# Performance work log

Hardware: AMD Instinct MI355X
Metric: run time of the kernel (lower is better)

The kernel has to match this reference:

```python
import jax, jax.numpy as jnp
import numpy as np

H = 300          # node_hidden_dim (GINE output dim)
D = 2 * H        # set2set in_channels = 600
STEPS = 2        # num_step_set2_set


def _lstm_cell(x, h, c, W_ih, W_hh, b_ih, b_hh):
    # PyTorch LSTM gate order: i, f, g, o
    gates = x @ W_ih.T + h @ W_hh.T + b_ih + b_hh
    i, f, g, o = jnp.split(gates, 4, axis=-1)
    c = jax.nn.sigmoid(f) * c + jax.nn.sigmoid(i) * jnp.tanh(g)
    h = jax.nn.sigmoid(o) * jnp.tanh(c)
    return h, c


def _set2set(x, batch, num_graphs, W_ih, W_hh, b_ih, b_hh):
    # torch_geometric Set2Set with processing_steps=STEPS, 1-layer LSTM
    B = num_graphs
    q_star = jnp.zeros((B, 2 * D), x.dtype)
    h = jnp.zeros((B, D), x.dtype)
    c = jnp.zeros((B, D), x.dtype)
    for _ in range(STEPS):
        h, c = _lstm_cell(q_star, h, c, W_ih, W_hh, b_ih, b_hh)
        q = h                                   # [B, D]
        e = jnp.sum(x * q[batch], axis=-1)      # [N]
        emax = jax.ops.segment_max(e, batch, num_segments=B)
        a = jnp.exp(e - emax[batch])
        asum = jax.ops.segment_sum(a, batch, num_segments=B)
        a = a / (asum[batch] + 1e-16)           # segment softmax
        r = jax.ops.segment_sum(a[:, None] * x, batch, num_segments=B)
        q_star = jnp.concatenate([q, r], axis=-1)   # [B, 2D]
    return q_star


def _l2norm(x):
    return x / jnp.maximum(jnp.linalg.norm(x, axis=1, keepdims=True), 1e-12)


def setup_inputs() -> dict:
    key = jax.random.key(0)
    ks = jax.random.split(key, 8)
    Nu, Nv, B = 8192, 8192, 256
    solute_x = jax.random.normal(ks[0], (Nu, H), jnp.float32)
    solvent_x = jax.random.normal(ks[1], (Nv, H), jnp.float32)
    solute_batch = jnp.sort(jax.random.randint(ks[2], (Nu,), 0, B)).astype(jnp.int32)
    solvent_batch = jnp.sort(jax.random.randint(ks[3], (Nv,), 0, B)).astype(jnp.int32)
    lstm_W_ih = jax.random.normal(ks[4], (4 * D, 2 * D), jnp.float32) * 0.02
    lstm_W_hh = jax.random.normal(ks[5], (4 * D, D), jnp.float32) * 0.02
    lstm_b_ih = jnp.zeros((4 * D,), jnp.float32)
    lstm_b_hh = jnp.zeros((4 * D,), jnp.float32)
    pred_W = jax.random.normal(ks[6], (1, 8 * H), jnp.float32) * 0.02
    pred_b = jnp.zeros((1,), jnp.float32)
    return {
        "solute_x": solute_x, "solvent_x": solvent_x,
        "solute_batch": solute_batch, "solvent_batch": solvent_batch,
        "num_graphs": B,
        "lstm_W_ih": lstm_W_ih, "lstm_W_hh": lstm_W_hh,
        "lstm_b_ih": lstm_b_ih, "lstm_b_hh": lstm_b_hh,
        "pred_W": pred_W, "pred_b": pred_b,
    }


def reference(solute_x, solvent_x, solute_batch, solvent_batch, num_graphs,
              lstm_W_ih, lstm_W_hh, lstm_b_ih, lstm_b_hh, pred_W, pred_b):
    # F.normalize(dim=1)
    su = _l2norm(solute_x)    # [Nu, H]
    sv = _l2norm(solvent_x)   # [Nv, H]
    # len_map = solute_len.T @ solvent_len == same-pair membership mask
    mask = (solute_batch[:, None] == solvent_batch[None, :]).astype(su.dtype)
    interaction_map = (su @ sv.T) * mask          # [Nu, Nv]
    ret_interaction_map = interaction_map
    solvent_prime = interaction_map.T @ su        # [Nv, H]
    solute_prime = interaction_map @ sv           # [Nu, H]
    su2 = jnp.concatenate([su, solute_prime], axis=1)    # [Nu, 2H]
    sv2 = jnp.concatenate([sv, solvent_prime], axis=1)   # [Nv, 2H]
    su_s2s = _set2set(su2, solute_batch, num_graphs, lstm_W_ih, lstm_W_hh, lstm_b_ih, lstm_b_hh)
    sv_s2s = _set2set(sv2, solvent_batch, num_graphs, lstm_W_ih, lstm_W_hh, lstm_b_ih, lstm_b_hh)
    final = jnp.concatenate([su_s2s, sv_s2s], axis=1)    # [B, 8H]
    predictions = final @ pred_W.T + pred_b              # [B, 1]
    return predictions, ret_interaction_map
```

## Files before the change

kernel.cpp:

```cpp
#include <hip/hip_runtime.h>
#include <math.h>

#define HDIM 300
#define DDIM 600
#define NGR  256

typedef float vf4 __attribute__((ext_vector_type(4)));
typedef float vf2 __attribute__((ext_vector_type(2)));

__device__ __forceinline__ float wred_sum(float v){
  #pragma unroll
  for(int o=32;o;o>>=1) v += __shfl_xor(v,o,64);
  return v;
}
__device__ __forceinline__ float wred_max(float v){
  #pragma unroll
  for(int o=32;o;o>>=1) v = fmaxf(v,__shfl_xor(v,o,64));
  return v;
}
__device__ __forceinline__ float sigm(float x){ return 1.f/(1.f+expf(-x)); }

__device__ __forceinline__ void fill_row(int i, const int* __restrict__ ub,
    const int* __restrict__ voff, float* __restrict__ mapbase, int Nv, int tid){
  int g = ub[i];
  int js = voff[g], je = voff[g+1];
  float* mrow = mapbase + (size_t)i*Nv;
  const vf4 z4 = {0.f,0.f,0.f,0.f};
  int nf4 = Nv >> 2;
  for (int q4=tid; q4<nf4; q4+=256){
    int j0 = q4*4;
    if (j0+4 <= js || j0 >= je){
      __builtin_nontemporal_store(z4, (vf4*)(mrow + j0));
    } else {
      #pragma unroll
      for(int u=0;u<4;u++){ int j=j0+u; if (j<js || j>=je) mrow[j]=0.f; }
    }
  }
}

__global__ __launch_bounds__(256) void k_norm_off(const float* __restrict__ xu,
    const float* __restrict__ xv, float* __restrict__ su, float* __restrict__ sv,
    int Nu, int Nv, const int* __restrict__ ub, const int* __restrict__ vb,
    int* __restrict__ uoff, int* __restrict__ voff,
    const float* __restrict__ b_ih, const float* __restrict__ b_hh,
    float* __restrict__ h1, float* __restrict__ c1,
    const float* __restrict__ pb, float* __restrict__ outp,
    const float* __restrict__ Wih, const float* __restrict__ Whh,
    float* __restrict__ gbase){
  int NBn = (Nu + Nv) >> 2;
  int b = blockIdx.x;
  int tid = threadIdx.x, lane = tid & 63, w = tid >> 6;
  if (b == NBn){
    int t = tid;
    if (t < NGR){
      int lo=0, hi=Nu;
      while(lo<hi){ int m=(lo+hi)>>1; if (ub[m] < t) lo=m+1; else hi=m; }
      uoff[t]=lo;
      lo=0; hi=Nv;
      while(lo<hi){ int m=(lo+hi)>>1; if (vb[m] < t) lo=m+1; else hi=m; }
      voff[t]=lo;
      if (t==0){ uoff[NGR]=Nu; voff[NGR]=Nv; }
      outp[t] = pb[0];
    }
    for (int d=tid; d<DDIM; d+=256){
      float gi = b_ih[d]      + b_hh[d];
      float gg = b_ih[1200+d] + b_hh[1200+d];
      float go = b_ih[1800+d] + b_hh[1800+d];
      float c  = sigm(gi)*tanhf(gg);
      c1[d]=c; h1[d]=sigm(go)*tanhf(c);
    }
    return;
  }
  if (b > NBn){
    __shared__ float h1l[DDIM];
    for (int d=tid; d<DDIM; d+=256){
      float gi = b_ih[d]      + b_hh[d];
      float gg = b_ih[1200+d] + b_hh[1200+d];
      float go = b_ih[1800+d] + b_hh[1800+d];
      float c  = sigm(gi)*tanhf(gg);
      h1l[d]   = sigm(go)*tanhf(c);
    }
    __syncthreads();
    int n = (b - NBn - 1)*4 + w;
    const float* wi = Wih + (size_t)n*1200;
    const float* wh = Whh + (size_t)n*600;
    float s = 0.f;
    for (int k=lane; k<DDIM; k+=64) s += h1l[k]*(wi[k] + wh[k]);
    s = wred_sum(s);
    if (lane==0) gbase[n] = s + b_ih[n] + b_hh[n];
    return;
  }
  int wid = b*4 + w;
  const float* src; float* dst;
  if (wid < Nu){ src = xu + (size_t)wid*HDIM; dst = su + (size_t)wid*HDIM; }
  else         { src = xv + (size_t)(wid-Nu)*HDIM; dst = sv + (size_t)(wid-Nu)*HDIM; }
  const vf4* s4 = (const vf4*)src;
  vf4 A = s4[lane];
  vf4 Bv = (lane<11)? s4[64+lane] : (vf4){0.f,0.f,0.f,0.f};
  float s = A.x*A.x+A.y*A.y+A.z*A.z+A.w*A.w + Bv.x*Bv.x+Bv.y*Bv.y+Bv.z*Bv.z+Bv.w*Bv.w;
  s = wred_sum(s);
  float inv = 1.f / fmaxf(sqrtf(s), 1e-12f);
  vf4* d4 = (vf4*)dst;
  d4[lane] = A*inv;
  if (lane<11) d4[64+lane] = Bv*inv;
}

__global__ __launch_bounds__(256) void k_prime(const float* __restrict__ su,
    const float* __restrict__ sv, const int* __restrict__ ub,
    const int* __restrict__ vb, const int* __restrict__ uoff,
    const int* __restrict__ voff, float* __restrict__ spr,
    float* __restrict__ svp, float* __restrict__ e1u, float* __restrict__ e1v,
    const float* __restrict__ h1, float* __restrict__ mapbase, int Nu, int Nv){
  int b = blockIdx.x;
  int tid = threadIdx.x, lane = tid & 63, w = tid >> 6;
  int r = b % 3;
  if (r == 2){ fill_row(b/3, ub, voff, mapbase, Nv, tid); return; }
  int idx = (b/3)*2 + r;
  bool isU = (idx < Nu);
  int i = isU ? idx : idx - Nu;
  const float* xa = isU ? su : sv;
  const float* xb = isU ? sv : su;
  const int* mybatch = isU ? ub : vb;
  const int* ooff    = isU ? voff : uoff;
  float* prime = isU ? spr : svp;
  float* eout  = isU ? e1u : e1v;

  __shared__ __align__(16) float xrow[304];
  __shared__ __align__(16) float prl[4*304];
  __shared__ float qv[2*HDIM];
  __shared__ float red[4];
  const float* rowp = xa + (size_t)i*HDIM;
  for (int t=tid; t<HDIM;   t+=256) xrow[t] = rowp[t];
  for (int t=tid; t<2*HDIM; t+=256) qv[t]   = h1[t];
  int g = mybatch[i];
  int js = ooff[g], je = ooff[g+1];
  __syncthreads();

  const vf4* x4 = (const vf4*)xrow;
  vf4 xA = x4[lane];
  vf4 xB = (lane<11)? x4[64+lane] : (vf4){0.f,0.f,0.f,0.f};
  vf4 prA = {0.f,0.f,0.f,0.f}, prB = {0.f,0.f,0.f,0.f};
  for (int j = js + w; j < je; j += 4){
    const vf4* orow = (const vf4*)(xb + (size_t)j*HDIM);
    vf4 oA = orow[lane];
    vf4 oB = (lane<11)? orow[64+lane] : (vf4){0.f,0.f,0.f,0.f};
    float d = oA.x*xA.x + oA.y*xA.y + oA.z*xA.z + oA.w*xA.w
            + oB.x*xB.x + oB.y*xB.y + oB.z*xB.z + oB.w*xB.w;
    d = wred_sum(d);
    if (isU && lane==0) mapbase[(size_t)i*Nv + j] = d;
    prA += d * oA;
    prB += d * oB;
  }
  vf4* p4 = (vf4*)(prl + w*304);
  p4[lane] = prA;
  if (lane<11) p4[64+lane] = prB;
  __syncthreads();
  float ep = 0.f;
  for (int t=tid; t<HDIM; t+=256){
    float s = prl[t] + prl[304+t] + prl[608+t] + prl[912+t];
    prime[(size_t)i*HDIM + t] = s;
    ep += xrow[t]*qv[t] + s*qv[HDIM+t];
  }
  ep = wred_sum(ep);
  if (lane==0) red[w] = ep;
  __syncthreads();
  if (tid==0) eout[i] = red[0]+red[1]+red[2]+red[3];
}

__global__ __launch_bounds__(256) void k_r1(const float* __restrict__ su,
    const float* __restrict__ sv, const float* __restrict__ spr,
    const float* __restrict__ svp, const float* __restrict__ e1u,
    const float* __restrict__ e1v, const int* __restrict__ uoff,
    const int* __restrict__ voff, float* __restrict__ r1){
  int tid = threadIdx.x, lane = tid & 63, w = tid >> 6;
  int bs = blockIdx.x; int set = bs >> 8; int g = bs & 255;
  const float* x  = set? sv  : su;
  const float* pr = set? svp : spr;
  const float* e  = set? e1v : e1u;
  const int* off  = set? voff: uoff;
  __shared__ float al[2048]; __shared__ float red[4]; __shared__ float shv;
  int ns = off[g], ne = off[g+1]; int n = ne - ns;
  float m = -INFINITY;
  for (int t=ns+tid; t<ne; t+=256) m = fmaxf(m, e[t]);
  m = wred_max(m);
  if (lane==0) red[w]=m;
  __syncthreads();
  if (tid==0) shv = fmaxf(fmaxf(red[0],red[1]),fmaxf(red[2],red[3]));
  __syncthreads();
  float emax = shv;
  float s = 0.f;
  for (int t=tid; t<n; t+=256){ float a = expf(e[ns+t]-emax); if (t<2048) al[t]=a; s += a; }
  s = wred_sum(s);
  __syncthreads();
  if (lane==0) red[w]=s;
  __syncthreads();
  if (tid==0) shv = red[0]+red[1]+red[2]+red[3];
  __syncthreads();
  float inv = 1.f/(shv + 1e-16f);
  float acc[3] = {0.f,0.f,0.f};
  for (int nn=0; nn<n; nn++){
    float a = (nn<2048)? al[nn] : expf(e[ns+nn]-emax);
    const float* xr = x  + (size_t)(ns+nn)*HDIM;
    const float* pp = pr + (size_t)(ns+nn)*HDIM;
    #pragma unroll
    for(int u=0;u<3;u++){ int c = tid + u*256; if (c<DDIM){
        float xv = (c<HDIM)? xr[c] : pp[c-HDIM]; acc[u] += a*xv; } }
  }
  #pragma unroll
  for(int u=0;u<3;u++){ int c = tid + u*256; if (c<DDIM) r1[(size_t)bs*DDIM + c] = acc[u]*inv; }
}

__global__ __launch_bounds__(256) void k_gemm_lstm(const float* __restrict__ r1,
    const float* __restrict__ Wih, const float* __restrict__ gbase,
    const float* __restrict__ c1, float* __restrict__ h2){
  __shared__ __align__(16) float smem[32*68];
  float* Al = smem;
  float* Bl = smem + 16*36;
  int tid = threadIdx.x;
  int d0  = blockIdx.x*16;
  int gs0 = blockIdx.y*32;
  int tx = tid & 15, ty = tid >> 4;
  float acc[2][4] = {};
  for (int kt=0; kt<600; kt+=16){
    int k = kt + tx;
    bool kok = (k < 600);
    #pragma unroll
    for (int u=0; u<2; u++){
      int rl = ty + u*16;
      Al[tx*36 + rl] = kok ? r1[(size_t)(gs0+rl)*DDIM + k] : 0.f;
    }
    #pragma unroll
    for (int u=0; u<4; u++){
      int cl = ty + u*16;
      int gate = cl >> 4, dd = cl & 15;
      int d = d0 + dd;
      Bl[tx*68 + cl] = (kok && d < 600)
          ? Wih[(size_t)(gate*600 + d)*1200 + 600 + k] : 0.f;
    }
    __syncthreads();
    #pragma unroll
    for (int kk=0; kk<16; kk++){
      vf2 av = ((const vf2*)(Al + kk*36))[ty];
      vf4 bv = ((const vf4*)(Bl + kk*68))[tx];
      float a[2]={av.x,av.y}, bb[4]={bv.x,bv.y,bv.z,bv.w};
      #pragma unroll
      for(int mm=0;mm<2;mm++)
        #pragma unroll
        for(int nn=0;nn<4;nn++) acc[mm][nn] += a[mm]*bb[nn];
    }
    __syncthreads();
  }
  #pragma unroll
  for (int mm=0; mm<2; mm++){
    vf4 o = {acc[mm][0], acc[mm][1], acc[mm][2], acc[mm][3]};
    ((vf4*)(smem + (ty*2+mm)*68))[tx] = o;
  }
  __syncthreads();
  int d_l = tid & 15, r0 = tid >> 4;
  int d = d0 + d_l;
  if (d < 600){
    float gb_i = gbase[d], gb_f = gbase[600+d], gb_g = gbase[1200+d], gb_o = gbase[1800+d];
    float cc1 = c1[d];
    #pragma unroll
    for (int u=0; u<2; u++){
      int rl = r0 + u*16;
      const float* gr = smem + rl*68;
      float gi = gr[d_l]      + gb_i;
      float gf = gr[16+d_l]   + gb_f;
      float gG = gr[32+d_l]   + gb_g;
      float go = gr[48+d_l]   + gb_o;
      float c  = sigm(gf)*cc1 + sigm(gi)*tanhf(gG);
      h2[(size_t)(gs0+rl)*DDIM + d] = sigm(go)*tanhf(c);
    }
  }
}

__global__ __launch_bounds__(256) void k_r2(const float* __restrict__ su,
    const float* __restrict__ sv, const float* __restrict__ spr,
    const float* __restrict__ svp, const int* __restrict__ uoff,
    const int* __restrict__ voff, const float* __restrict__ h2,
    const float* __restrict__ pW, float* __restrict__ e2u,
    float* __restrict__ e2v, float* __restrict__ outp){
  int tid = threadIdx.x, lane = tid & 63, w = tid >> 6;
  int bs = blockIdx.x; int set = bs >> 8; int g = bs & 255;
  const float* x  = set? sv  : su;
  const float* pr = set? svp : spr;
  const int* off  = set? voff: uoff;
  float* e2g      = set? e2v : e2u;
  __shared__ float q[DDIM]; __shared__ float e2l[128]; __shared__ float al[128];
  __shared__ float red[4]; __shared__ float shv;
  for (int t=tid; t<DDIM; t+=256) q[t] = h2[(size_t)bs*DDIM + t];
  int ns = off[g], ne = off[g+1]; int n = ne - ns;
  __syncthreads();
  for (int node = ns + w; node < ne; node += 4){
    const float* xr = x  + (size_t)node*HDIM;
    const float* pp = pr + (size_t)node*HDIM;
    float d = 0.f;
    #pragma unroll
    for(int c=0;c<10;c++){ int k = lane + 64*c; if (k<DDIM){
        float xv = (k<HDIM)? xr[k] : pp[k-HDIM]; d += xv*q[k]; } }
    d = wred_sum(d);
    if (lane==0){ int t = node-ns; if (t<128) e2l[t] = d; else e2g[node] = d; }
  }
  __syncthreads();
  float m = -INFINITY;
  for (int t=tid; t<n; t+=256) m = fmaxf(m, (t<128)? e2l[t] : e2g[ns+t]);
  m = wred_max(m);
  if (lane==0) red[w]=m;
  __syncthreads();
  if (tid==0) shv = fmaxf(fmaxf(red[0],red[1]),fmaxf(red[2],red[3]));
  __syncthreads();
  float emax = shv;
  float s = 0.f;
  for (int t=tid; t<n; t+=256){
    float a = expf(((t<128)? e2l[t] : e2g[ns+t]) - emax);
    if (t<128) al[t]=a; else e2g[ns+t]=a;
    s += a;
  }
  s = wred_sum(s);
  __syncthreads();
  if (lane==0) red[w]=s;
  __syncthreads();
  if (tid==0) shv = red[0]+red[1]+red[2]+red[3];
  __syncthreads();
  float inv = 1.f/(shv + 1e-16f);
  float acc[3] = {0.f,0.f,0.f};
  for (int nn=0; nn<n; nn++){
    float a = (nn<128)? al[nn] : e2g[ns+nn];
    const float* xr = x  + (size_t)(ns+nn)*HDIM;
    const float* pp = pr + (size_t)(ns+nn)*HDIM;
    #pragma unroll
    for(int u=0;u<3;u++){ int c = tid + u*256; if (c<DDIM){
        float xv = (c<HDIM)? xr[c] : pp[c-HDIM]; acc[u] += a*xv; } }
  }
  int hoff = set? 1200 : 0;
  float p = 0.f;
  #pragma unroll
  for(int u=0;u<3;u++){ int c = tid + u*256; if (c<DDIM) p += (acc[u]*inv)*pW[hoff+600+c]; }
  for (int t=tid; t<DDIM; t+=256) p += q[t]*pW[hoff+t];
  p = wred_sum(p);
  __syncthreads();
  if (lane==0) red[w] = p;
  __syncthreads();
  if (tid==0) atomicAdd(&outp[g], red[0]+red[1]+red[2]+red[3]);
}

extern "C" void kernel_launch(void* const* d_in, const int* in_sizes, int n_in,
                              void* d_out, int out_size, void* d_ws, size_t ws_size,
                              hipStream_t stream) {
  const float* solute_x  = (const float*)d_in[0];
  const float* solvent_x = (const float*)d_in[1];
  const int*   ub        = (const int*)d_in[2];
  const int*   vb        = (const int*)d_in[3];
  const float* Wih  = (const float*)d_in[5];
  const float* Whh  = (const float*)d_in[6];
  const float* b_ih = (const float*)d_in[7];
  const float* b_hh = (const float*)d_in[8];
  const float* pW   = (const float*)d_in[9];
  const float* pb   = (const float*)d_in[10];

  int Nu = in_sizes[0] / HDIM;
  int Nv = in_sizes[1] / HDIM;

  float* out = (float*)d_out;
  int predn = out_size - Nu*Nv;
  float* mapbase = out + predn;

  float* ws = (float*)d_ws;
  float* su    = ws;
  float* sv    = su    + (size_t)Nu*HDIM;
  float* spr   = sv    + (size_t)Nv*HDIM;
  float* svp   = spr   + (size_t)Nu*HDIM;
  float* e1u   = svp   + (size_t)Nv*HDIM;
  float* e1v   = e1u   + Nu;
  float* h1    = e1v   + Nv;
  float* c1    = h1    + DDIM;
  float* r1    = c1    + DDIM;
  float* gbase = r1    + 512*DDIM;
  float* h2    = gbase + 2400;
  int*   uoff  = (int*)(h2 + 512*DDIM);
  int*   voff  = uoff + 257;

  k_norm_off<<<dim3((Nu+Nv)/4 + 1 + 600), dim3(256), 0, stream>>>(
      solute_x, solvent_x, su, sv, Nu, Nv, ub, vb, uoff, voff,
      b_ih, b_hh, h1, c1, pb, out, Wih, Whh, gbase);
  k_prime<<<dim3(24576), dim3(256), 0, stream>>>(
      su, sv, ub, vb, uoff, voff, spr, svp, e1u, e1v, h1, mapbase, Nu, Nv);
  k_r1<<<dim3(512), dim3(256), 0, stream>>>(
      su, sv, spr, svp, e1u, e1v, uoff, voff, r1);
  k_gemm_lstm<<<dim3(38, 16), dim3(256), 0, stream>>>(r1, Wih, gbase, c1, h2);
  k_r2<<<dim3(512), dim3(256), 0, stream>>>(
      su, sv, spr, svp, uoff, voff, h2, pW, e1u, e1v, out);
}
```

Baseline: 524.6 us.

## Spread interaction-map zero-fill rows across prime, r1 and r2 kernels

Before, the 8192 zero-fill rows of the interaction map were all interleaved into k_prime. Now k_prime fills 5461 rows, and the remaining rows are split between k_r1 and k_r2 as extra blocks, assigned with a proportional interleaving helper. The aim is to hide the bandwidth-bound map writes behind the small, latency-bound r1 and r2 kernels, which launch only 512 blocks each. The cost is extra blocks in those kernels and a risk of contending with their memory traffic.

```diff
diff --git a/kernel.cpp b/kernel.cpp
--- a/kernel.cpp
+++ b/kernel.cpp
@@ -36,6 +36,13 @@
       for(int u=0;u<4;u++){ int j=j0+u; if (j<js || j>=je) mrow[j]=0.f; }
     }
   }
+}
+
+__device__ __forceinline__ int split_cf(int b, int C, int G, int* fi){
+  unsigned ci = (unsigned)(((unsigned long long)b * (unsigned)C) / (unsigned)G);
+  unsigned cn = (unsigned)(((unsigned long long)(b+1) * (unsigned)C) / (unsigned)G);
+  if (cn == ci){ *fi = b - (int)ci; return -1; }
+  return (int)ci;
 }
 
 __global__ __launch_bounds__(256) void k_norm_off(const float* __restrict__ xu,
@@ -111,11 +118,10 @@
     const int* __restrict__ voff, float* __restrict__ spr,
     float* __restrict__ svp, float* __restrict__ e1u, float* __restrict__ e1v,
     const float* __restrict__ h1, float* __restrict__ mapbase, int Nu, int Nv){
-  int b = blockIdx.x;
   int tid = threadIdx.x, lane = tid & 63, w = tid >> 6;
-  int r = b % 3;
-  if (r == 2){ fill_row(b/3, ub, voff, mapbase, Nv, tid); return; }
-  int idx = (b/3)*2 + r;
+  int fi;
+  int idx = split_cf(blockIdx.x, 16384, 21845, &fi);
+  if (idx < 0){ fill_row(fi, ub, voff, mapbase, Nv, tid); return; }
   bool isU = (idx < Nu);
   int i = isU ? idx : idx - Nu;
   const float* xa = isU ? su : sv;
@@ -171,9 +177,13 @@
     const float* __restrict__ sv, const float* __restrict__ spr,
     const float* __restrict__ svp, const float* __restrict__ e1u,
     const float* __restrict__ e1v, const int* __restrict__ uoff,
-    const int* __restrict__ voff, float* __restrict__ r1){
+    const int* __restrict__ voff, float* __restrict__ r1,
+    const int* __restrict__ ub, float* __restrict__ mapbase, int Nv){
   int tid = threadIdx.x, lane = tid & 63, w = tid >> 6;
-  int bs = blockIdx.x; int set = bs >> 8; int g = bs & 255;
+  int fi;
+  int bs = split_cf(blockIdx.x, 512, 1877, &fi);
+  if (bs < 0){ fill_row(5461 + fi, ub, voff, mapbase, Nv, tid); return; }
+  int set = bs >> 8; int g = bs & 255;
   const float* x  = set? sv  : su;
   const float* pr = set? svp : spr;
   const float* e  = set? e1v : e1u;
@@ -280,9 +290,13 @@
     const float* __restrict__ svp, const int* __restrict__ uoff,
     const int* __restrict__ voff, const float* __restrict__ h2,
     const float* __restrict__ pW, float* __restrict__ e2u,
-    float* __restrict__ e2v, float* __restrict__ outp){
+    float* __restrict__ e2v, float* __restrict__ outp,
+    const int* __restrict__ ub, float* __restrict__ mapbase, int Nv){
   int tid = threadIdx.x, lane = tid & 63, w = tid >> 6;
-  int bs = blockIdx.x; int set = bs >> 8; int g = bs & 255;
+  int fi;
+  int bs = split_cf(blockIdx.x, 512, 1878, &fi);
+  if (bs < 0){ fill_row(6826 + fi, ub, voff, mapbase, Nv, tid); return; }
+  int set = bs >> 8; int g = bs & 255;
   const float* x  = set? sv  : su;
   const float* pr = set? svp : spr;
   const int* off  = set? voff: uoff;
@@ -384,11 +398,11 @@
   k_norm_off<<<dim3((Nu+Nv)/4 + 1 + 600), dim3(256), 0, stream>>>(
       solute_x, solvent_x, su, sv, Nu, Nv, ub, vb, uoff, voff,
       b_ih, b_hh, h1, c1, pb, out, Wih, Whh, gbase);
-  k_prime<<<dim3(24576), dim3(256), 0, stream>>>(
+  k_prime<<<dim3(21845), dim3(256), 0, stream>>>(
       su, sv, ub, vb, uoff, voff, spr, svp, e1u, e1v, h1, mapbase, Nu, Nv);
-  k_r1<<<dim3(512), dim3(256), 0, stream>>>(
-      su, sv, spr, svp, e1u, e1v, uoff, voff, r1);
+  k_r1<<<dim3(1877), dim3(256), 0, stream>>>(
+      su, sv, spr, svp, e1u, e1v, uoff, voff, r1, ub, mapbase, Nv);
   k_gemm_lstm<<<dim3(38, 16), dim3(256), 0, stream>>>(r1, Wih, gbase, c1, h2);
-  k_r2<<<dim3(512), dim3(256), 0, stream>>>(
-      su, sv, spr, svp, uoff, voff, h2, pW, e1u, e1v, out);
-}
+  k_r2<<<dim3(1878), dim3(256), 0, stream>>>(
+      su, sv, spr, svp, uoff, voff, h2, pW, e1u, e1v, out, ub, mapbase, Nv);
+}
```

New measurement: 537.0 us. 2.4% more time.
